# Kernel optimization log

Hardware: AMD Instinct MI355X
Metric: run time of the kernel (lower is better)

The kernel has to match this reference:

```python
import jax, jax.numpy as jnp
import numpy as np

N = 64      # hippo_n (state size)
H = 512     # input_size (channels)
L = 2048    # sequence_length


def _hippo_dplr(n):
    # make_HiPPO -> make_NPLR_HiPPO -> make_DPLR_HiPPO (numpy, deterministic)
    pr = np.sqrt(1 + 2 * np.arange(n))
    a = pr[:, None] * pr[None, :]
    a = np.tril(a) - np.diag(np.arange(n))
    a = -a
    p = np.sqrt(np.arange(n) + 0.5)
    b = np.sqrt(2 * np.arange(n) + 1.0)
    s = a + p[:, None] * p[None, :]
    s_diag = np.diagonal(s)
    lam_real = np.mean(s_diag) * np.ones_like(s_diag)
    lam_imag, v = np.linalg.eigh(s * -1j)
    p = v.conj().T @ p
    b = v.conj().T @ b
    return lam_real, lam_imag, p, b


def setup_inputs() -> dict:
    key = jax.random.key(0)
    k_u, k_c, k_step = jax.random.split(key, 3)
    lam_r, lam_i, p, b = _hippo_dplr(N)
    tile = lambda x: jnp.tile(jnp.asarray(x, dtype=jnp.float32), (H, 1))
    dt_min, dt_max = 0.001, 0.1
    log_step = jax.random.uniform(k_step, (H, 1)) * (
        jnp.log(dt_max) - jnp.log(dt_min)) + jnp.log(dt_min)
    return {
        "u": jax.random.normal(k_u, (L, H), dtype=jnp.float32),
        "lambda_real": tile(lam_r),
        "lambda_imag": tile(lam_i),
        "p_real": tile(p.real),
        "p_imag": tile(p.imag),
        "b_real": tile(b.real),
        "b_imag": tile(b.imag),
        "c": jax.random.normal(k_c, (H, N, 2), dtype=jnp.float32) * 0.5 ** 0.5,
        "d": jnp.ones((H, 1), dtype=jnp.float32),
        "log_step": log_step.astype(jnp.float32),
    }


def _s4_convolve(u, lambda_real, lambda_imag, p_real, p_imag,
                 b_real, b_imag, c, d, log_step):
    # u: (L, H); params: (H, N) / (H, N, 2) / (H, 1)
    lam = jnp.clip(lambda_real, None, -0.0001) + 1j * lambda_imag   # (H, N)
    pc = p_real + 1j * p_imag                                        # (H, N)
    bc = b_real + 1j * b_imag                                        # (H, N)
    cc = (c[..., 0] + 1j * c[..., 1]).conj()                         # aterm[0]
    qc = pc.conj()                                                   # aterm[1]
    step = jnp.exp(log_step)                                         # (H, 1)

    Ls = u.shape[0]
    omega = jnp.exp(-2j * jnp.pi * (jnp.arange(Ls) / Ls))            # (L,)
    g = (2.0 / step) * ((1.0 - omega) / (1.0 + omega))[None, :]      # (H, L)
    c2 = 2.0 / (1.0 + omega)                                         # (L,)

    # Shared Cauchy denominator: (H, L, N)
    denom = 1.0 / (g[:, :, None] - lam[:, None, :])
    k00 = jnp.einsum("hn,hln->hl", cc * bc, denom)
    k01 = jnp.einsum("hn,hln->hl", cc * pc, denom)
    k10 = jnp.einsum("hn,hln->hl", qc * bc, denom)
    k11 = jnp.einsum("hn,hln->hl", qc * pc, denom)
    roots = c2[None, :] * (k00 - k01 * (1.0 / (1.0 + k11)) * k10)    # (H, L)
    kern = jnp.fft.ifft(roots, Ls, axis=-1).real                     # (H, L)

    # FFT convolution (fft=True path)
    uT = u.T                                                         # (H, L)
    ud = jnp.fft.rfft(jnp.pad(uT, ((0, 0), (0, Ls))), axis=-1)
    Kd = jnp.fft.rfft(jnp.pad(kern, ((0, 0), (0, Ls))), axis=-1)
    conv = jnp.fft.irfft(ud * Kd, axis=-1)[:, :Ls]                   # (H, L)
    return (conv + d * uT).T                                         # (L, H)


def reference(u, lambda_real, lambda_imag, p_real, p_imag,
              b_real, b_imag, c, d, log_step):
    return _s4_convolve(u, lambda_real, lambda_imag, p_real, p_imag,
                        b_real, b_imag, c, d, log_step)
```

## Files before the change

### kernel.cpp

```cpp
#include <hip/hip_runtime.h>
#include <math.h>

#define L_SEQ 2048
#define H_CH  512
#define N_ST  64

__device__ __forceinline__ float frcp(float x) { return __builtin_amdgcn_rcpf(x); }
#define A2(i) ((i) + ((i) >> 4))

template<int LOGN, int ST0 = 0>
__device__ __forceinline__ void fft_lds(float2* buf, const float2* tw,
                                        int tid, float ssign)
{
    constexpr int N   = 1 << LOGN;
    constexpr int NBF = N / 512;
#pragma unroll
    for (int st = ST0; st < LOGN; ++st) {
        const int h2s = (N >> 1) >> st;
#pragma unroll
        for (int bq = 0; bq < NBF; ++bq) {
            const int b  = tid + bq * 256;
            const int j  = b & (h2s - 1);
            const int i0 = ((b >> (LOGN - 1 - st)) << (LOGN - st)) + j;
            const int i1 = i0 + h2s;
            const float2 uu = buf[A2(i0)];
            const float2 vv = buf[A2(i1)];
            const float2 w  = tw[A2((j << st) << (11 - LOGN))];
            const float  wy = ssign * w.y;
            buf[A2(i0)] = make_float2(uu.x + vv.x, uu.y + vv.y);
            const float d0 = uu.x - vv.x, d1 = uu.y - vv.y;
            buf[A2(i1)] = make_float2(d0 * w.x - d1 * wy, d0 * wy + d1 * w.x);
        }
        __syncthreads();
    }
}

__global__ __launch_bounds__(256)
void s4_prep(const float* __restrict__ lam_r_g, const float* __restrict__ lam_i_g,
             const float* __restrict__ p_r_g,  const float* __restrict__ p_i_g,
             const float* __restrict__ b_r_g,  const float* __restrict__ b_i_g,
             const float* __restrict__ c_g,
             float4* __restrict__ Wa, float4* __restrict__ Wb, float* __restrict__ Wc)
{
    const int g = blockIdx.x * 256 + threadIdx.x;
    const float lr = fminf(lam_r_g[g], -0.0001f);
    const float li = lam_i_g[g];
    const float pr = p_r_g[g], pi = p_i_g[g];
    const float br = b_r_g[g], bi = b_i_g[g];
    const float c0 = c_g[2 * g], c1 = c_g[2 * g + 1];
    Wa[g] = make_float4(lr, li, c0 * br + c1 * bi, c0 * bi - c1 * br);
    Wb[g] = make_float4(c0 * pr + c1 * pi, c0 * pi - c1 * pr,
                        pr * br + pi * bi, pr * bi - pi * br);
    Wc[g] = pr * pr + pi * pi;
}

__global__ __launch_bounds__(256)
void s4_fftconv(const float4* __restrict__ Wa, const float4* __restrict__ Wb,
                const float* __restrict__ Wc, const float* __restrict__ log_step_g,
                const float* __restrict__ u, float* __restrict__ Y)
{
    __shared__ float2 bufK[2175];
    __shared__ float2 bufU[2175];
    __shared__ float2 tw[1087];
    const int h   = blockIdx.x;
    const int tid = threadIdx.x;
    float2* __restrict__ rbuf = bufU;

    for (int k = tid; k < 1024; k += 256) {
        float sv, cv;
        sincosf((float)k * (6.2831853071795864769f / 2048.0f), &sv, &cv);
        tw[A2(k)] = make_float2(cv, sv);
    }

    const float step = expf(log_step_g[h]);
    const float ts   = 2.0f / step;
    const float4* __restrict__ wa = Wa + h * N_ST;
    const float4* __restrict__ wb = Wb + h * N_ST;
    const float*  __restrict__ wc = Wc + h * N_ST;

    for (int pass = 0; pass < 2; ++pass) {
        float grq[4], giq[4], c2rq[4], c2iq[4];
#pragma unroll
        for (int q = 0; q < 4; ++q) {
            const int l = tid + q * 256 + pass * 1024;
            float wi, wr;
            sincosf(-6.2831853071795864769f * ((float)l * (1.0f / (float)L_SEQ)),
                    &wi, &wr);
            const float dr = 1.0f + wr, di = wi;
            const float dv = frcp(dr * dr + di * di);
            const float nr = 1.0f - wr, ni = -wi;
            grq[q]  = ts * (nr * dr + ni * di) * dv;
            giq[q]  = ts * (ni * dr - nr * di) * dv;
            c2rq[q] = 2.0f * dr * dv;
            c2iq[q] = -2.0f * di * dv;
        }
        float s00r[4] = {0,0,0,0}, s00i[4] = {0,0,0,0};
        float s01r[4] = {0,0,0,0}, s01i[4] = {0,0,0,0};
        float s10r[4] = {0,0,0,0}, s10i[4] = {0,0,0,0};
        float s11r[4] = {0,0,0,0}, s11i[4] = {0,0,0,0};
#pragma unroll 4
        for (int n = 0; n < N_ST; ++n) {
            const float4 A = wa[n];
            const float4 B = wb[n];
            const float w11 = wc[n];
#pragma unroll
            for (int q = 0; q < 4; ++q) {
                const float ddr = grq[q] - A.x;
                const float ddi = giq[q] - A.y;
                const float rinv = frcp(fmaf(ddr, ddr, ddi * ddi));
                const float rr = ddr * rinv;
                const float ri = -ddi * rinv;
                s00r[q] = fmaf(A.z, rr, fmaf(-A.w, ri, s00r[q]));
                s00i[q] = fmaf(A.z, ri, fmaf( A.w, rr, s00i[q]));
                s01r[q] = fmaf(B.x, rr, fmaf(-B.y, ri, s01r[q]));
                s01i[q] = fmaf(B.x, ri, fmaf( B.y, rr, s01i[q]));
                s10r[q] = fmaf(B.z, rr, fmaf(-B.w, ri, s10r[q]));
                s10i[q] = fmaf(B.z, ri, fmaf( B.w, rr, s10i[q]));
                s11r[q] = fmaf(w11, rr, s11r[q]);
                s11i[q] = fmaf(w11, ri, s11i[q]);
            }
        }
#pragma unroll
        for (int q = 0; q < 4; ++q) {
            const float qdr = 1.0f + s11r[q], qdi = s11i[q];
            const float qinv = frcp(qdr * qdr + qdi * qdi);
            const float pnr = s01r[q] * s10r[q] - s01i[q] * s10i[q];
            const float pni = s01r[q] * s10i[q] + s01i[q] * s10r[q];
            const float qr = (pnr * qdr + pni * qdi) * qinv;
            const float qi = (pni * qdr - pnr * qdi) * qinv;
            const float rr0 = s00r[q] - qr, ri0 = s00i[q] - qi;
            rbuf[tid + q * 256 + pass * 1024] =
                make_float2(c2rq[q] * rr0 - c2iq[q] * ri0,
                            c2rq[q] * ri0 + c2iq[q] * rr0);
        }
    }

    float uv[8];
#pragma unroll
    for (int q = 0; q < 4; ++q) {
        const int t = tid + q * 256;
        uv[q]     = u[t * H_CH + h];
        uv[q + 4] = u[(t + 1024) * H_CH + h];
    }

    __syncthreads();

#pragma unroll
    for (int q = 0; q < 4; ++q) {
        const int k = tid + q * 256;
        float zr, zi;
        if (k == 0) {
            const float X0 = rbuf[0].x, XM = rbuf[1024].x;
            zr = X0 + XM;  zi = X0 - XM;
        } else {
            const float2 a  = rbuf[k],        b2 = rbuf[2048 - k];
            const float2 a2 = rbuf[1024 - k], b3 = rbuf[1024 + k];
            const float xkr = 0.5f * (a.x + b2.x),  xki = 0.5f * (a.y - b2.y);
            const float xmr = 0.5f * (a2.x + b3.x), xmi = -0.5f * (a2.y - b3.y);
            const float er = xkr + xmr, ei = xki + xmi;
            const float o_r = xkr - xmr, o_i = xki - xmi;
            const float2 w = tw[A2(k)];
            zr = er - fmaf(w.x, o_i,  w.y * o_r);
            zi = ei + fmaf(w.x, o_r, -w.y * o_i);
        }
        bufK[A2(k)] = make_float2(zr, zi);
    }
    __syncthreads();
    fft_lds<10>(bufK, tw, tid, 1.0f);

    float2 v0[4];
#pragma unroll
    for (int q = 0; q < 4; ++q) {
        const int t  = tid + q * 256;
        const int n0 = t >> 1;
        const float2 za = bufK[A2(__brev(n0) >> 22)];
        const float2 zb = bufK[A2(__brev(512 + n0) >> 22)];
        const float k0v = ((t & 1) ? za.y : za.x) * (1.0f / 2048.0f);
        const float k1v = ((t & 1) ? zb.y : zb.x) * (1.0f / 2048.0f);
        v0[q] = make_float2(k0v, k1v);
    }
    __syncthreads();
#pragma unroll
    for (int q = 0; q < 4; ++q) {
        const int t = tid + q * 256;
        const float2 v = v0[q];
        const float2 w = tw[A2(t)];
        bufK[A2(t)] = v;
        bufK[A2(t + 1024)] = make_float2(fmaf(v.x, w.x,  v.y * w.y),
                                         fmaf(v.y, w.x, -v.x * w.y));
    }
    __syncthreads();
    fft_lds<11, 1>(bufK, tw, tid, -1.0f);

#pragma unroll
    for (int q = 0; q < 4; ++q) {
        const int t = tid + q * 256;
        const float2 v = make_float2(uv[q], uv[q + 4]);
        const float2 w = tw[A2(t)];
        bufU[A2(t)] = v;
        bufU[A2(t + 1024)] = make_float2(fmaf(v.x, w.x,  v.y * w.y),
                                         fmaf(v.y, w.x, -v.x * w.y));
    }
    __syncthreads();
    fft_lds<11, 1>(bufU, tw, tid, -1.0f);

    float2 R[8];
#pragma unroll
    for (int q = 0; q < 8; ++q) {
        const int m  = tid + q * 256;
        const int mp = (2048 - m) & 2047;
        const int bm = __brev(m)  >> 21;
        const int bp = __brev(mp) >> 21;
        const float2 Zk  = bufK[A2(bm)], Zkp = bufK[A2(bp)];
        const float2 Zu  = bufU[A2(bm)], Zup = bufU[A2(bp)];
        const float F0r = 0.5f * (Zk.x + Zkp.x), F0i = 0.5f * (Zk.y - Zkp.y);
        const float F1r = 0.5f * (Zk.y + Zkp.y), F1i = 0.5f * (Zkp.x - Zk.x);
        const float U0r = 0.5f * (Zu.x + Zup.x), U0i = 0.5f * (Zu.y - Zup.y);
        const float U1r = 0.5f * (Zu.y + Zup.y), U1i = 0.5f * (Zup.x - Zu.x);
        const float Pr = F0r * U0r - F0i * U0i;
        const float Pi = F0r * U0i + F0i * U0r;
        const float Qr = F0r * U1r - F0i * U1i + F1r * U0r - F1i * U0i;
        const float Qi = F0r * U1i + F0i * U1r + F1r * U0i + F1i * U0r;
        R[q] = make_float2(Pr - Qi, Pi + Qr);
    }
    __syncthreads();
#pragma unroll
    for (int q = 0; q < 8; ++q) bufK[A2(tid + q * 256)] = R[q];
    __syncthreads();
    fft_lds<11>(bufK, tw, tid, 1.0f);

#pragma unroll
    for (int q = 0; q < 4; ++q) {
        const int t = tid + q * 256;
        const float2 rl = bufK[A2(__brev(t)        >> 21)];
        const float2 rh = bufK[A2(__brev(t + 1024) >> 21)];
        Y[h * 2048 + t]        = rl.x * (1.0f / 2048.0f);
        Y[h * 2048 + 1024 + t] = (rh.x + rl.y) * (1.0f / 2048.0f);
    }
}

__global__ __launch_bounds__(256)
void s4_finish(const float* __restrict__ Y, const float* __restrict__ u,
               const float* __restrict__ dvec, float* __restrict__ out)
{
    __shared__ float tile[64][65];
    const int t0   = blockIdx.x * 64;
    const int h0   = blockIdx.y * 64;
    const int lane = threadIdx.x & 63;
    const int rowg = threadIdx.x >> 6;

#pragma unroll
    for (int rr = 0; rr < 16; ++rr) {
        const int hr = rowg * 16 + rr;
        tile[hr][lane] = Y[(h0 + hr) * 2048 + t0 + lane];
    }
    __syncthreads();

    const float dh = dvec[h0 + lane];
#pragma unroll
    for (int rr = 0; rr < 16; ++rr) {
        const int tr = rowg * 16 + rr;
        const int t  = t0 + tr;
        out[t * H_CH + h0 + lane] =
            fmaf(dh, u[t * H_CH + h0 + lane], tile[lane][tr]);
    }
}

extern "C" void kernel_launch(void* const* d_in, const int* in_sizes, int n_in,
                              void* d_out, int out_size, void* d_ws, size_t ws_size,
                              hipStream_t stream)
{
    const float* u        = (const float*)d_in[0];
    const float* lam_r    = (const float*)d_in[1];
    const float* lam_i    = (const float*)d_in[2];
    const float* p_r      = (const float*)d_in[3];
    const float* p_i      = (const float*)d_in[4];
    const float* b_r      = (const float*)d_in[5];
    const float* b_i      = (const float*)d_in[6];
    const float* cmat     = (const float*)d_in[7];
    const float* dvec     = (const float*)d_in[8];
    const float* log_step = (const float*)d_in[9];
    float* out = (float*)d_out;

    char* ws = (char*)d_ws;
    float*  Y     = (float*)(ws + (size_t)8 * 1024 * 1024);
    float4* Wa    = (float4*)(ws + (size_t)12 * 1024 * 1024);
    float4* Wb    = (float4*)(ws + (size_t)12 * 1024 * 1024 + 512 * 1024);
    float*  Wc    = (float*) (ws + (size_t)13 * 1024 * 1024);

    s4_prep<<<dim3(H_CH * N_ST / 256), dim3(256), 0, stream>>>(
        lam_r, lam_i, p_r, p_i, b_r, b_i, cmat, Wa, Wb, Wc);
    s4_fftconv<<<dim3(H_CH), dim3(256), 0, stream>>>(
        Wa, Wb, Wc, log_step, u, Y);
    s4_finish<<<dim3(L_SEQ / 64, H_CH / 64), dim3(256), 0, stream>>>(
        Y, u, dvec, out);
}
```

Baseline: 70.67 us.

## Use 512-thread blocks for per-channel FFT convolution kernel

```diff
diff --git a/kernel.cpp b/kernel.cpp
--- a/kernel.cpp
+++ b/kernel.cpp
@@ -4,6 +4,7 @@
 #define L_SEQ 2048
 #define H_CH  512
 #define N_ST  64
+#define BLK   512
 
 __device__ __forceinline__ float frcp(float x) { return __builtin_amdgcn_rcpf(x); }
 #define A2(i) ((i) + ((i) >> 4))
@@ -13,13 +14,13 @@
                                         int tid, float ssign)
 {
     constexpr int N   = 1 << LOGN;
-    constexpr int NBF = N / 512;
+    constexpr int NBF = (N / 2) / BLK;
 #pragma unroll
     for (int st = ST0; st < LOGN; ++st) {
         const int h2s = (N >> 1) >> st;
 #pragma unroll
         for (int bq = 0; bq < NBF; ++bq) {
-            const int b  = tid + bq * 256;
+            const int b  = tid + bq * BLK;
             const int j  = b & (h2s - 1);
             const int i0 = ((b >> (LOGN - 1 - st)) << (LOGN - st)) + j;
             const int i1 = i0 + h2s;
@@ -54,7 +55,7 @@
     Wc[g] = pr * pr + pi * pi;
 }
 
-__global__ __launch_bounds__(256)
+__global__ __launch_bounds__(BLK)
 void s4_fftconv(const float4* __restrict__ Wa, const float4* __restrict__ Wb,
                 const float* __restrict__ Wc, const float* __restrict__ log_step_g,
                 const float* __restrict__ u, float* __restrict__ Y)
@@ -66,7 +67,17 @@
     const int tid = threadIdx.x;
     float2* __restrict__ rbuf = bufU;
 
-    for (int k = tid; k < 1024; k += 256) {
+    float uv[4];
+#pragma unroll
+    for (int q = 0; q < 2; ++q) {
+        const int t = tid + q * BLK;
+        uv[q]     = u[t * H_CH + h];
+        uv[q + 2] = u[(t + 1024) * H_CH + h];
+    }
+
+#pragma unroll
+    for (int q = 0; q < 2; ++q) {
+        const int k = tid + q * BLK;
         float sv, cv;
         sincosf((float)k * (6.2831853071795864769f / 2048.0f), &sv, &cv);
         tw[A2(k)] = make_float2(cv, sv);
@@ -78,11 +89,11 @@
     const float4* __restrict__ wb = Wb + h * N_ST;
     const float*  __restrict__ wc = Wc + h * N_ST;
 
-    for (int pass = 0; pass < 2; ++pass) {
+    {
         float grq[4], giq[4], c2rq[4], c2iq[4];
 #pragma unroll
         for (int q = 0; q < 4; ++q) {
-            const int l = tid + q * 256 + pass * 1024;
+            const int l = tid + q * BLK;
             float wi, wr;
             sincosf(-6.2831853071795864769f * ((float)l * (1.0f / (float)L_SEQ)),
                     &wi, &wr);
@@ -129,25 +140,17 @@
             const float qr = (pnr * qdr + pni * qdi) * qinv;
             const float qi = (pni * qdr - pnr * qdi) * qinv;
             const float rr0 = s00r[q] - qr, ri0 = s00i[q] - qi;
-            rbuf[tid + q * 256 + pass * 1024] =
+            rbuf[tid + q * BLK] =
                 make_float2(c2rq[q] * rr0 - c2iq[q] * ri0,
                             c2rq[q] * ri0 + c2iq[q] * rr0);
         }
     }
 
-    float uv[8];
-#pragma unroll
-    for (int q = 0; q < 4; ++q) {
-        const int t = tid + q * 256;
-        uv[q]     = u[t * H_CH + h];
-        uv[q + 4] = u[(t + 1024) * H_CH + h];
-    }
-
-    __syncthreads();
-
-#pragma unroll
-    for (int q = 0; q < 4; ++q) {
-        const int k = tid + q * 256;
+    __syncthreads();
+
+#pragma unroll
+    for (int q = 0; q < 2; ++q) {
+        const int k = tid + q * BLK;
         float zr, zi;
         if (k == 0) {
             const float X0 = rbuf[0].x, XM = rbuf[1024].x;
@@ -168,10 +171,10 @@
     __syncthreads();
     fft_lds<10>(bufK, tw, tid, 1.0f);
 
-    float2 v0[4];
-#pragma unroll
-    for (int q = 0; q < 4; ++q) {
-        const int t  = tid + q * 256;
+    float2 v0[2];
+#pragma unroll
+    for (int q = 0; q < 2; ++q) {
+        const int t  = tid + q * BLK;
         const int n0 = t >> 1;
         const float2 za = bufK[A2(__brev(n0) >> 22)];
         const float2 zb = bufK[A2(__brev(512 + n0) >> 22)];
@@ -181,8 +184,8 @@
     }
     __syncthreads();
 #pragma unroll
-    for (int q = 0; q < 4; ++q) {
-        const int t = tid + q * 256;
+    for (int q = 0; q < 2; ++q) {
+        const int t = tid + q * BLK;
         const float2 v = v0[q];
         const float2 w = tw[A2(t)];
         bufK[A2(t)] = v;
@@ -193,9 +196,9 @@
     fft_lds<11, 1>(bufK, tw, tid, -1.0f);
 
 #pragma unroll
-    for (int q = 0; q < 4; ++q) {
-        const int t = tid + q * 256;
-        const float2 v = make_float2(uv[q], uv[q + 4]);
+    for (int q = 0; q < 2; ++q) {
+        const int t = tid + q * BLK;
+        const float2 v = make_float2(uv[q], uv[q + 2]);
         const float2 w = tw[A2(t)];
         bufU[A2(t)] = v;
         bufU[A2(t + 1024)] = make_float2(fmaf(v.x, w.x,  v.y * w.y),
@@ -204,10 +207,10 @@
     __syncthreads();
     fft_lds<11, 1>(bufU, tw, tid, -1.0f);
 
-    float2 R[8];
-#pragma unroll
-    for (int q = 0; q < 8; ++q) {
-        const int m  = tid + q * 256;
+    float2 R[4];
+#pragma unroll
+    for (int q = 0; q < 4; ++q) {
+        const int m  = tid + q * BLK;
         const int mp = (2048 - m) & 2047;
         const int bm = __brev(m)  >> 21;
         const int bp = __brev(mp) >> 21;
@@ -225,13 +228,13 @@
     }
     __syncthreads();
 #pragma unroll
-    for (int q = 0; q < 8; ++q) bufK[A2(tid + q * 256)] = R[q];
+    for (int q = 0; q < 4; ++q) bufK[A2(tid + q * BLK)] = R[q];
     __syncthreads();
     fft_lds<11>(bufK, tw, tid, 1.0f);
 
 #pragma unroll
-    for (int q = 0; q < 4; ++q) {
-        const int t = tid + q * 256;
+    for (int q = 0; q < 2; ++q) {
+        const int t = tid + q * BLK;
         const float2 rl = bufK[A2(__brev(t)        >> 21)];
         const float2 rh = bufK[A2(__brev(t + 1024) >> 21)];
         Y[h * 2048 + t]        = rl.x * (1.0f / 2048.0f);
@@ -290,7 +293,7 @@
 
     s4_prep<<<dim3(H_CH * N_ST / 256), dim3(256), 0, stream>>>(
         lam_r, lam_i, p_r, p_i, b_r, b_i, cmat, Wa, Wb, Wc);
-    s4_fftconv<<<dim3(H_CH), dim3(256), 0, stream>>>(
+    s4_fftconv<<<dim3(H_CH), dim3(BLK), 0, stream>>>(
         Wa, Wb, Wc, log_step, u, Y);
     s4_finish<<<dim3(L_SEQ / 64, H_CH / 64), dim3(256), 0, stream>>>(
         Y, u, dvec, out);
```

After: 61.86 us. 1.14x faster.
